# Optimization experiments

Measured on AMD Instinct MI355X. Metric: run time of the kernel, lower is better.

## Reference

```python
import math
import jax, jax.numpy as jnp
import numpy as np

N = 100000      # nodes
E = 3200000     # edges (avg degree 32)
NFEAT = 512
NH = 256
NC = 40
NL = 8
ALPHA = 0.1
LAMDA = 0.5


def setup_inputs() -> dict:
    key = jax.random.key(0)
    ks = jax.random.split(key, 9)
    features = jax.random.normal(ks[0], (N, NFEAT), jnp.float32)
    edge_rows = jax.random.randint(ks[1], (E,), 0, N, jnp.int32)
    edge_cols = jax.random.randint(ks[2], (E,), 0, N, jnp.int32)
    # scale by 1/avg_degree so aggregated features stay O(1) (mimics normalized adjacency)
    edge_vals = jax.random.uniform(ks[3], (E,), jnp.float32) / 32.0
    # fcs[0]: nn.Linear(nfeat, nhidden) default init U(-1/sqrt(in), 1/sqrt(in))
    b1 = 1.0 / math.sqrt(NFEAT)
    W_in = jax.random.uniform(ks[4], (NFEAT, NH), jnp.float32, -b1, b1)
    b_in = jax.random.uniform(ks[5], (NH,), jnp.float32, -b1, b1)
    # GraphConvolution weights: U(-1/sqrt(out), 1/sqrt(out))
    bw = 1.0 / math.sqrt(NH)
    conv_weights = jax.random.uniform(ks[6], (NL, NH, NH), jnp.float32, -bw, bw)
    # fcs[1]: nn.Linear(nhidden, nclass)
    b2 = 1.0 / math.sqrt(NH)
    W_out = jax.random.uniform(ks[7], (NH, NC), jnp.float32, -b2, b2)
    b_out = jax.random.uniform(ks[8], (NC,), jnp.float32, -b2, b2)
    return {
        "features": features,
        "edge_rows": edge_rows,
        "edge_cols": edge_cols,
        "edge_vals": edge_vals,
        "W_in": W_in,
        "b_in": b_in,
        "conv_weights": conv_weights,
        "W_out": W_out,
        "b_out": b_out,
    }


def reference(features, edge_rows, edge_cols, edge_vals, W_in, b_in, conv_weights, W_out, b_out):
    # dropout p=0 in eval -> identity
    h = jax.nn.relu(features @ W_in + b_in)  # [N, NH]
    h0 = h
    for i in range(NL):
        theta = math.log(LAMDA / (i + 1) + 1.0)
        # SpMM: hi = G @ h via gather + segment-sum over destination rows
        hi = jax.ops.segment_sum(edge_vals[:, None] * h[edge_cols], edge_rows, num_segments=N)
        support = (1.0 - ALPHA) * hi + ALPHA * h0  # variant=False -> r == support
        h = jax.nn.relu(theta * (support @ conv_weights[i]) + (1.0 - theta) * support)
    return h @ W_out + b_out  # [N, NC]
```

## Files before the change

kernel.cpp:

```cpp
#include <hip/hip_runtime.h>
#include <hip/hip_fp16.h>
#include <math.h>

#define NNODE   100000
#define NEDGE   3200000
#define NFEAT   512
#define NH      256
#define NC      40
#define NL      8

#define SCAN_B  256

typedef _Float16 f16x8 __attribute__((ext_vector_type(8)));
typedef float    f32x4 __attribute__((ext_vector_type(4)));

__global__ void count_deg_kernel(const int* __restrict__ rows, int* __restrict__ deg, int e) {
    int i = blockIdx.x * blockDim.x + threadIdx.x;
    if (i < e) atomicAdd(&deg[rows[i]], 1);
}

__global__ void scan_pass1(const int* __restrict__ deg, int* __restrict__ rowptr,
                           int* __restrict__ bsums, int n) {
    __shared__ int sm[SCAN_B];
    int i = blockIdx.x * SCAN_B + threadIdx.x;
    int v = (i < n) ? deg[i] : 0;
    sm[threadIdx.x] = v;
    __syncthreads();
    for (int off = 1; off < SCAN_B; off <<= 1) {
        int t = (threadIdx.x >= (unsigned)off) ? sm[threadIdx.x - off] : 0;
        __syncthreads();
        sm[threadIdx.x] += t;
        __syncthreads();
    }
    if (i < n) rowptr[i] = sm[threadIdx.x] - v;
    if (threadIdx.x == SCAN_B - 1) bsums[blockIdx.x] = sm[threadIdx.x];
}

__global__ void scan_pass2(int* __restrict__ bsums, int nb) {
    __shared__ int sm[512];
    int tid = threadIdx.x;
    int v = (tid < nb) ? bsums[tid] : 0;
    sm[tid] = v;
    __syncthreads();
    for (int off = 1; off < 512; off <<= 1) {
        int t = (tid >= off) ? sm[tid - off] : 0;
        __syncthreads();
        sm[tid] += t;
        __syncthreads();
    }
    if (tid < nb) bsums[tid] = sm[tid] - v;
}

__global__ void scan_pass3(int* __restrict__ rowptr, const int* __restrict__ bsums,
                           int* __restrict__ cursor, int n, int total) {
    int i = blockIdx.x * blockDim.x + threadIdx.x;
    if (i < n) {
        int v = rowptr[i] + bsums[i / SCAN_B];
        rowptr[i] = v;
        cursor[i] = v;
    }
    if (i == 0) rowptr[n] = total;
}

__global__ void scatter_edges_kernel(const int* __restrict__ rows, const int* __restrict__ cols,
                                     const float* __restrict__ vals, int* __restrict__ cursor,
                                     unsigned* __restrict__ csr_pk, int e) {
    int i = blockIdx.x * blockDim.x + threadIdx.x;
    if (i < e) {
        int r = rows[i];
        int p = atomicAdd(&cursor[r], 1);
        int q = (int)rintf(vals[i] * 1048576.0f);
        if (q > 32767) q = 32767;
        csr_pk[p] = ((unsigned)cols[i] << 15) | (unsigned)q;
    }
}

__device__ inline float4 dec8(uint2 p) {
    __half2 h01 = *(__half2*)&p.x;
    __half2 h23 = *(__half2*)&p.y;
    float2 f01 = __half22float2(h01);
    float2 f23 = __half22float2(h23);
    return make_float4(f01.x, f01.y, f23.x, f23.y);
}

__device__ inline void gload16(const void* g, void* l) {
    __builtin_amdgcn_global_load_lds((const __attribute__((address_space(1))) void*)g,
                                     (__attribute__((address_space(3))) void*)l,
                                     16, 0, 0);
}

#define VAL_SCALE 9.5367431640625e-7f

__global__ void convert_win(const float* __restrict__ in, __half* __restrict__ out) {
    int idx = blockIdx.x * blockDim.x + threadIdx.x;
    if (idx < NFEAT * NH) {
        int k = idx >> 8;
        int n = idx & 255;
        out[n * NFEAT + k] = __float2half(in[idx]);
    }
}

__global__ void convert_convw(const float* __restrict__ in, __half* __restrict__ out) {
    int idx = blockIdx.x * blockDim.x + threadIdx.x;
    if (idx < NL * NH * NH) {
        int l = idx >> 16;
        int rem = idx & 65535;
        int k = rem >> 8;
        int n = rem & 255;
        out[(size_t)l * 65536 + n * 256 + k] = __float2half(in[idx]);
    }
}

__global__ void convert_wout(const float* __restrict__ in, __half* __restrict__ out) {
    int idx = blockIdx.x * blockDim.x + threadIdx.x;
    if (idx < 64 * 256) {
        int ncol = idx >> 8;
        int k    = idx & 255;
        out[idx] = (ncol < NC) ? __float2half(in[k * NC + ncol]) : __float2half(0.f);
    }
}

__global__ __launch_bounds__(256) void spmm_full(
    const int* __restrict__ rowptr, const unsigned* __restrict__ csr_pk,
    const __half* __restrict__ h16, const __half* __restrict__ h016,
    __half* __restrict__ sup16, int n)
{
    int lane = threadIdx.x & 63;
    int r = blockIdx.x * 4 + (threadIdx.x >> 6);
    if (r >= n) return;
    int e0 = rowptr[r], e1 = rowptr[r + 1];
    const uint2* hv = (const uint2*)h16;
    float4 acc = make_float4(0.f, 0.f, 0.f, 0.f);
    int e = e0;
    #pragma unroll 1
    for (; e + 8 <= e1; e += 8) {
        unsigned a[8];
        uint2 p[8];
        #pragma unroll
        for (int j = 0; j < 8; ++j) a[j] = csr_pk[e + j];
        #pragma unroll
        for (int j = 0; j < 8; ++j) p[j] = hv[(size_t)(a[j] >> 15) * 64 + lane];
        #pragma unroll
        for (int j = 0; j < 8; ++j) {
            float v = (float)(a[j] & 32767u) * VAL_SCALE;
            float4 x = dec8(p[j]);
            acc.x += v * x.x; acc.y += v * x.y;
            acc.z += v * x.z; acc.w += v * x.w;
        }
    }
    #pragma unroll 1
    for (; e < e1; ++e) {
        unsigned a = csr_pk[e];
        float v = (float)(a & 32767u) * VAL_SCALE;
        float4 x = dec8(hv[(size_t)(a >> 15) * 64 + lane]);
        acc.x += v * x.x; acc.y += v * x.y; acc.z += v * x.z; acc.w += v * x.w;
    }
    float4 s0 = dec8(((const uint2*)h016)[(size_t)r * 64 + lane]);
    float4 o;
    o.x = 0.9f * acc.x + 0.1f * s0.x;
    o.y = 0.9f * acc.y + 0.1f * s0.y;
    o.z = 0.9f * acc.z + 0.1f * s0.z;
    o.w = 0.9f * acc.w + 0.1f * s0.w;
    __half2 ha = __floats2half2_rn(o.x, o.y);
    __half2 hb = __floats2half2_rn(o.z, o.w);
    uint2 pk;
    pk.x = *(unsigned*)&ha;
    pk.y = *(unsigned*)&hb;
    ((uint2*)sup16)[(size_t)r * 64 + lane] = pk;
}

__global__ __launch_bounds__(256) void spmm_half(
    const int* __restrict__ rowptr, const unsigned* __restrict__ csr_pk,
    const __half* __restrict__ h16, const __half* __restrict__ h016,
    __half* __restrict__ sup16, int n, int uoff)
{
    int lane = threadIdx.x & 63;
    int r = blockIdx.x * 4 + (threadIdx.x >> 6);
    if (r >= n) return;
    int e0 = rowptr[r], e1 = rowptr[r + 1];
    const unsigned* hv = (const unsigned*)h16;
    float2 acc = make_float2(0.f, 0.f);
    int e = e0;
    #pragma unroll 1
    for (; e + 8 <= e1; e += 8) {
        unsigned a[8], p[8];
        #pragma unroll
        for (int j = 0; j < 8; ++j) a[j] = csr_pk[e + j];
        #pragma unroll
        for (int j = 0; j < 8; ++j) p[j] = hv[(size_t)(a[j] >> 15) * 128 + uoff + lane];
        #pragma unroll
        for (int j = 0; j < 8; ++j) {
            float v = (float)(a[j] & 32767u) * VAL_SCALE;
            float2 x = __half22float2(*(__half2*)&p[j]);
            acc.x += v * x.x; acc.y += v * x.y;
        }
    }
    #pragma unroll 1
    for (; e < e1; ++e) {
        unsigned a = csr_pk[e];
        float v = (float)(a & 32767u) * VAL_SCALE;
        unsigned pw = hv[(size_t)(a >> 15) * 128 + uoff + lane];
        float2 x = __half22float2(*(__half2*)&pw);
        acc.x += v * x.x; acc.y += v * x.y;
    }
    unsigned s0w = ((const unsigned*)h016)[(size_t)r * 128 + uoff + lane];
    float2 s0 = __half22float2(*(__half2*)&s0w);
    float2 o;
    o.x = 0.9f * acc.x + 0.1f * s0.x;
    o.y = 0.9f * acc.y + 0.1f * s0.y;
    __half2 hh = __floats2half2_rn(o.x, o.y);
    ((unsigned*)sup16)[(size_t)r * 128 + uoff + lane] = *(unsigned*)&hh;
}

template <bool AFLOAT>
__global__ __launch_bounds__(512) void mfma_gemm(
    const void* __restrict__ Aptr, const __half* __restrict__ BT,
    const float* __restrict__ bias, const __half* __restrict__ Csrc16,
    __half* __restrict__ out16, int M, int K,
    float theta, float omt, int mode)
{
    __shared__ __align__(16) char smem[49152];
    const int tid  = threadIdx.x;
    const int lane = tid & 63;
    const int w    = tid >> 6;
    const int wr   = w >> 2;
    const int wc   = w & 3;
    const int bm0  = blockIdx.x * 128;
    const size_t strideB = (size_t)K * 2;

    f32x4 acc[4][4];
    #pragma unroll
    for (int m = 0; m < 4; ++m)
        #pragma unroll
        for (int n = 0; n < 4; ++n)
            acc[m][n] = (f32x4)0.f;

    auto stage = [&](int kt, int buf) {
        char* base = smem + buf * 24576;
        const long k0b = (long)kt * 64;
        if constexpr (AFLOAT) {
            const float* A32 = (const float*)Aptr;
            #pragma unroll
            for (int it = 0; it < 2; ++it) {
                int idx = tid + it * 512;
                int r   = idx >> 3;
                int t   = idx & 7;
                int grow = bm0 + r; if (grow >= M) grow = M - 1;
                float4 f = *(const float4*)&A32[(size_t)grow * K + kt * 32 + t * 4];
                __half2 a = __floats2half2_rn(f.x, f.y);
                __half2 b = __floats2half2_rn(f.z, f.w);
                uint2 pk;
                pk.x = *(unsigned*)&a;
                pk.y = *(unsigned*)&b;
                int slot = t >> 1;
                int off  = r * 64 + ((slot ^ ((r >> 1) & 3)) << 4) + (t & 1) * 8;
                *(uint2*)(base + off) = pk;
            }
        } else {
            const char* A16 = (const char*)Aptr;
            int row = w * 16 + (lane >> 2);
            int q   = (lane & 3) * 16;
            int qs  = q ^ (((row >> 1) & 3) << 4);
            int grow = bm0 + row; if (grow >= M) grow = M - 1;
            gload16(A16 + (size_t)grow * strideB + k0b + qs, base + w * 1024);
        }
        #pragma unroll
        for (int i = 0; i < 2; ++i) {
            int ia  = w * 2 + i;
            int row = ia * 16 + (lane >> 2);
            int q   = (lane & 3) * 16;
            int qs  = q ^ (((row >> 1) & 3) << 4);
            gload16((const char*)BT + (size_t)row * strideB + k0b + qs,
                    base + 8192 + ia * 1024);
        }
    };

    auto compute = [&](int buf) {
        const char* As = smem + buf * 24576;
        const char* Bs = As + 8192;
        const int q = (lane >> 4) * 16;
        f16x8 af[4], bf[4];
        #pragma unroll
        for (int m = 0; m < 4; ++m) {
            int row = wr * 64 + m * 16 + (lane & 15);
            af[m] = *(const f16x8*)(As + row * 64 + (q ^ (((row >> 1) & 3) << 4)));
        }
        #pragma unroll
        for (int n = 0; n < 4; ++n) {
            int col = wc * 64 + n * 16 + (lane & 15);
            bf[n] = *(const f16x8*)(Bs + col * 64 + (q ^ (((col >> 1) & 3) << 4)));
        }
        #pragma unroll
        for (int m = 0; m < 4; ++m)
            #pragma unroll
            for (int n = 0; n < 4; ++n)
                acc[m][n] = __builtin_amdgcn_mfma_f32_16x16x32_f16(af[m], bf[n], acc[m][n], 0, 0, 0);
    };

    const int nkt = K >> 5;
    stage(0, 0);
    __syncthreads();
    for (int kt = 0; kt < nkt; ++kt) {
        if (kt + 1 < nkt) stage(kt + 1, (kt + 1) & 1);
        compute(kt & 1);
        __syncthreads();
    }

    #pragma unroll
    for (int m = 0; m < 4; ++m) {
        int rbase = bm0 + wr * 64 + m * 16 + (lane >> 4) * 4;
        #pragma unroll
        for (int r = 0; r < 4; ++r) {
            int grow = rbase + r;
            if (grow >= M) continue;
            #pragma unroll
            for (int n = 0; n < 4; ++n) {
                int gcol = wc * 64 + n * 16 + (lane & 15);
                float x = acc[m][n][r];
                if (mode == 0) {
                    x = fmaxf(x + bias[gcol], 0.f);
                } else {
                    float s = __half2float(Csrc16[(size_t)grow * 256 + gcol]);
                    x = fmaxf(theta * x + omt * s, 0.f);
                }
                out16[(size_t)grow * 256 + gcol] = __float2half(x);
            }
        }
    }
}

__global__ __launch_bounds__(256) void mfma_out(
    const __half* __restrict__ A16, const __half* __restrict__ BT,
    const float* __restrict__ bias, float* __restrict__ out32, int M)
{
    __shared__ __align__(16) char smem[40960];
    const int tid  = threadIdx.x;
    const int lane = tid & 63;
    const int w    = tid >> 6;
    const int bm0  = blockIdx.x * 256;

    f32x4 acc[4][4];
    #pragma unroll
    for (int m = 0; m < 4; ++m)
        #pragma unroll
        for (int n = 0; n < 4; ++n)
            acc[m][n] = (f32x4)0.f;

    auto stage = [&](int kt, int buf) {
        char* base = smem + buf * 20480;
        const long k0b = (long)kt * 64;
        #pragma unroll
        for (int i = 0; i < 4; ++i) {
            int ia  = w * 4 + i;
            int row = ia * 16 + (lane >> 2);
            int q   = (lane & 3) * 16;
            int qs  = q ^ (((row >> 1) & 3) << 4);
            int grow = bm0 + row; if (grow >= M) grow = M - 1;
            gload16((const char*)A16 + (size_t)grow * 512 + k0b + qs, base + ia * 1024);
        }
        {
            int row = w * 16 + (lane >> 2);
            int q   = (lane & 3) * 16;
            int qs  = q ^ (((row >> 1) & 3) << 4);
            gload16((const char*)BT + (size_t)row * 512 + k0b + qs,
                    base + 16384 + w * 1024);
        }
    };

    auto compute = [&](int buf) {
        const char* As = smem + buf * 20480;
        const char* Bs = As + 16384;
        const int q = (lane >> 4) * 16;
        f16x8 af[4], bf[4];
        #pragma unroll
        for (int m = 0; m < 4; ++m) {
            int row = w * 64 + m * 16 + (lane & 15);
            af[m] = *(const f16x8*)(As + row * 64 + (q ^ (((row >> 1) & 3) << 4)));
        }
        #pragma unroll
        for (int n = 0; n < 4; ++n) {
            int col = n * 16 + (lane & 15);
            bf[n] = *(const f16x8*)(Bs + col * 64 + (q ^ (((col >> 1) & 3) << 4)));
        }
        #pragma unroll
        for (int m = 0; m < 4; ++m)
            #pragma unroll
            for (int n = 0; n < 4; ++n)
                acc[m][n] = __builtin_amdgcn_mfma_f32_16x16x32_f16(af[m], bf[n], acc[m][n], 0, 0, 0);
    };

    stage(0, 0);
    __syncthreads();
    for (int kt = 0; kt < 8; ++kt) {
        if (kt + 1 < 8) stage(kt + 1, (kt + 1) & 1);
        compute(kt & 1);
        __syncthreads();
    }

    #pragma unroll
    for (int m = 0; m < 4; ++m) {
        int rbase = bm0 + w * 64 + m * 16 + (lane >> 4) * 4;
        #pragma unroll
        for (int r = 0; r < 4; ++r) {
            int grow = rbase + r;
            if (grow >= M) continue;
            #pragma unroll
            for (int n = 0; n < 3; ++n) {
                int gcol = n * 16 + (lane & 15);
                if (gcol < NC)
                    out32[(size_t)grow * NC + gcol] = acc[m][n][r] + bias[gcol];
            }
        }
    }
}

extern "C" void kernel_launch(void* const* d_in, const int* in_sizes, int n_in,
                              void* d_out, int out_size, void* d_ws, size_t ws_size,
                              hipStream_t stream) {
    const float* features = (const float*)d_in[0];
    const int*   erows    = (const int*)d_in[1];
    const int*   ecols    = (const int*)d_in[2];
    const float* evals    = (const float*)d_in[3];
    const float* W_in     = (const float*)d_in[4];
    const float* b_in     = (const float*)d_in[5];
    const float* convW    = (const float*)d_in[6];
    const float* W_out    = (const float*)d_in[7];
    const float* b_out    = (const float*)d_in[8];
    float* out = (float*)d_out;

    const int n = NNODE;
    const int e = NEDGE;

    char* w = (char*)d_ws;
    auto alloc = [&](size_t bytes) -> void* {
        void* p = (void*)w;
        w += (bytes + 255) & ~(size_t)255;
        return p;
    };
    __half*   h0_16    = (__half*)alloc((size_t)n * NH * 2);
    __half*   hb_16    = (__half*)alloc((size_t)n * NH * 2);
    __half*   sup16    = (__half*)alloc((size_t)n * NH * 2);
    __half*   WtIn16   = (__half*)alloc((size_t)NFEAT * NH * 2);
    __half*   convWt16 = (__half*)alloc((size_t)NL * NH * NH * 2);
    __half*   WtOut16  = (__half*)alloc((size_t)64 * NH * 2);
    int*      rowptr   = (int*)alloc((size_t)(n + 1) * 4);
    int*      cursor   = (int*)alloc((size_t)n * 4);
    int*      bsums    = (int*)alloc(4096 * 4);
    unsigned* csr_pk   = (unsigned*)alloc((size_t)e * 4);

    convert_win<<<(NFEAT * NH + 255) / 256, 256, 0, stream>>>(W_in, WtIn16);
    convert_convw<<<(NL * NH * NH + 255) / 256, 256, 0, stream>>>(convW, convWt16);
    convert_wout<<<(64 * 256 + 255) / 256, 256, 0, stream>>>(W_out, WtOut16);

    hipMemsetAsync(cursor, 0, (size_t)n * 4, stream);
    count_deg_kernel<<<(e + 255) / 256, 256, 0, stream>>>(erows, cursor, e);
    int nb = (n + SCAN_B - 1) / SCAN_B;
    scan_pass1<<<nb, SCAN_B, 0, stream>>>(cursor, rowptr, bsums, n);
    scan_pass2<<<1, 512, 0, stream>>>(bsums, nb);
    scan_pass3<<<nb, SCAN_B, 0, stream>>>(rowptr, bsums, cursor, n, e);
    scatter_edges_kernel<<<(e + 255) / 256, 256, 0, stream>>>(
        erows, ecols, evals, cursor, csr_pk, e);

    dim3 gmm((n + 127) / 128, 1);
    mfma_gemm<true><<<gmm, 512, 0, stream>>>(features, WtIn16, b_in, nullptr,
                                             h0_16, n, NFEAT, 0.f, 0.f, 0);

    const __half* hcur16 = h0_16;
    for (int i = 0; i < NL; ++i) {
        if ((i & 1) == 0) {
            spmm_full<<<(n + 3) / 4, 256, 0, stream>>>(rowptr, csr_pk,
                                                       hcur16, h0_16, sup16, n);
        } else {
            spmm_half<<<(n + 3) / 4, 256, 0, stream>>>(rowptr, csr_pk,
                                                       hcur16, h0_16, sup16, n, 0);
            spmm_half<<<(n + 3) / 4, 256, 0, stream>>>(rowptr, csr_pk,
                                                       hcur16, h0_16, sup16, n, 64);
        }
        double th = log(0.5 / (double)(i + 1) + 1.0);
        mfma_gemm<false><<<gmm, 512, 0, stream>>>(sup16, convWt16 + (size_t)i * NH * NH,
                                                  nullptr, sup16, hb_16,
                                                  n, NH, (float)th, (float)(1.0 - th), 1);
        hcur16 = hb_16;
    }

    mfma_out<<<(n + 255) / 256, 256, 0, stream>>>(hb_16, WtOut16, b_out, out, n);
}
```

Baseline: 2.923 ms.

## Bucket CSR edges by column block and sweep SpMM rows per column band

Edges are now sorted within each row into 25 column buckets of 4096 nodes, which requires a per-row, per-bucket count, scan and scatter. A new SpMM kernel gives each wavefront 25 rows and walks all of them through one column bucket at a time, so that gathers from the feature matrix stay inside a small band that can stay cache-resident. Every layer now uses two half-width launches instead of alternating full and half kernels. The price is a larger preprocessing cost, 25 register accumulators per lane, and loss of the 8-way unrolled gather loop, since each row-bucket segment holds only about one edge and the latency is poorly hidden.

Result: slower. 8.657 ms (+196.2%).

```diff
diff --git a/kernel.cpp b/kernel.cpp
--- a/kernel.cpp
+++ b/kernel.cpp
@@ -10,20 +10,32 @@
 #define NL      8
 
 #define SCAN_B  256
+#define NB      25
+#define RPW     25
+#define RPB     100
+#define PBLK    1024
 
 typedef _Float16 f16x8 __attribute__((ext_vector_type(8)));
 typedef float    f32x4 __attribute__((ext_vector_type(4)));
 
-__global__ void count_deg_kernel(const int* __restrict__ rows, int* __restrict__ deg, int e) {
+#define VAL_SCALE 9.5367431640625e-7f
+
+__global__ void cnt2_kernel(const int* __restrict__ rows, const int* __restrict__ cols,
+                            int* __restrict__ cnt2, int e) {
     int i = blockIdx.x * blockDim.x + threadIdx.x;
-    if (i < e) atomicAdd(&deg[rows[i]], 1);
-}
-
-__global__ void scan_pass1(const int* __restrict__ deg, int* __restrict__ rowptr,
+    if (i < e) atomicAdd(&cnt2[rows[i] * NB + (cols[i] >> 12)], 1);
+}
+
+__global__ void scan_pass1(const int* __restrict__ cnt2, int* __restrict__ rowptr,
                            int* __restrict__ bsums, int n) {
     __shared__ int sm[SCAN_B];
     int i = blockIdx.x * SCAN_B + threadIdx.x;
-    int v = (i < n) ? deg[i] : 0;
+    int v = 0;
+    if (i < n) {
+        const int* c = &cnt2[i * NB];
+        #pragma unroll
+        for (int b = 0; b < NB; ++b) v += c[b];
+    }
     sm[threadIdx.x] = v;
     __syncthreads();
     for (int off = 1; off < SCAN_B; off <<= 1) {
@@ -51,27 +63,39 @@
     if (tid < nb) bsums[tid] = sm[tid] - v;
 }
 
-__global__ void scan_pass3(int* __restrict__ rowptr, const int* __restrict__ bsums,
-                           int* __restrict__ cursor, int n, int total) {
+__global__ void scan_pass3(int* __restrict__ rowptr, const int* __restrict__ bsums, int n) {
     int i = blockIdx.x * blockDim.x + threadIdx.x;
-    if (i < n) {
-        int v = rowptr[i] + bsums[i / SCAN_B];
-        rowptr[i] = v;
-        cursor[i] = v;
-    }
-    if (i == 0) rowptr[n] = total;
-}
-
-__global__ void scatter_edges_kernel(const int* __restrict__ rows, const int* __restrict__ cols,
-                                     const float* __restrict__ vals, int* __restrict__ cursor,
-                                     unsigned* __restrict__ csr_pk, int e) {
+    if (i < n) rowptr[i] += bsums[i / SCAN_B];
+}
+
+__global__ void rowptr2_kernel(const int* __restrict__ rowptr, const int* __restrict__ cnt2,
+                               int* __restrict__ rowptr2, int* __restrict__ cursor2,
+                               int n, int e) {
+    int r = blockIdx.x * blockDim.x + threadIdx.x;
+    if (r < n) {
+        int run = rowptr[r];
+        const int* c = &cnt2[r * NB];
+        #pragma unroll
+        for (int b = 0; b < NB; ++b) {
+            rowptr2[r * NB + b] = run;
+            cursor2[r * NB + b] = run;
+            run += c[b];
+        }
+    }
+    if (r == 0) rowptr2[(size_t)n * NB] = e;
+}
+
+__global__ void scatter2_kernel(const int* __restrict__ rows, const int* __restrict__ cols,
+                                const float* __restrict__ vals, int* __restrict__ cursor2,
+                                unsigned* __restrict__ csr_pk, int e) {
     int i = blockIdx.x * blockDim.x + threadIdx.x;
     if (i < e) {
         int r = rows[i];
-        int p = atomicAdd(&cursor[r], 1);
+        int c = cols[i];
+        int p = atomicAdd(&cursor2[r * NB + (c >> 12)], 1);
         int q = (int)rintf(vals[i] * 1048576.0f);
         if (q > 32767) q = 32767;
-        csr_pk[p] = ((unsigned)cols[i] << 15) | (unsigned)q;
+        csr_pk[p] = ((unsigned)c << 15) | (unsigned)q;
     }
 }
 
@@ -88,8 +112,6 @@
                                      (__attribute__((address_space(3))) void*)l,
                                      16, 0, 0);
 }
-
-#define VAL_SCALE 9.5367431640625e-7f
 
 __global__ void convert_win(const float* __restrict__ in, __half* __restrict__ out) {
     int idx = blockIdx.x * blockDim.x + threadIdx.x;
@@ -120,96 +142,61 @@
     }
 }
 
-__global__ __launch_bounds__(256) void spmm_full(
-    const int* __restrict__ rowptr, const unsigned* __restrict__ csr_pk,
-    const __half* __restrict__ h16, const __half* __restrict__ h016,
-    __half* __restrict__ sup16, int n)
-{
-    int lane = threadIdx.x & 63;
-    int r = blockIdx.x * 4 + (threadIdx.x >> 6);
-    if (r >= n) return;
-    int e0 = rowptr[r], e1 = rowptr[r + 1];
-    const uint2* hv = (const uint2*)h16;
-    float4 acc = make_float4(0.f, 0.f, 0.f, 0.f);
-    int e = e0;
-    #pragma unroll 1
-    for (; e + 8 <= e1; e += 8) {
-        unsigned a[8];
-        uint2 p[8];
-        #pragma unroll
-        for (int j = 0; j < 8; ++j) a[j] = csr_pk[e + j];
-        #pragma unroll
-        for (int j = 0; j < 8; ++j) p[j] = hv[(size_t)(a[j] >> 15) * 64 + lane];
-        #pragma unroll
-        for (int j = 0; j < 8; ++j) {
-            float v = (float)(a[j] & 32767u) * VAL_SCALE;
-            float4 x = dec8(p[j]);
-            acc.x += v * x.x; acc.y += v * x.y;
-            acc.z += v * x.z; acc.w += v * x.w;
-        }
-    }
-    #pragma unroll 1
-    for (; e < e1; ++e) {
-        unsigned a = csr_pk[e];
-        float v = (float)(a & 32767u) * VAL_SCALE;
-        float4 x = dec8(hv[(size_t)(a >> 15) * 64 + lane]);
-        acc.x += v * x.x; acc.y += v * x.y; acc.z += v * x.z; acc.w += v * x.w;
-    }
-    float4 s0 = dec8(((const uint2*)h016)[(size_t)r * 64 + lane]);
-    float4 o;
-    o.x = 0.9f * acc.x + 0.1f * s0.x;
-    o.y = 0.9f * acc.y + 0.1f * s0.y;
-    o.z = 0.9f * acc.z + 0.1f * s0.z;
-    o.w = 0.9f * acc.w + 0.1f * s0.w;
-    __half2 ha = __floats2half2_rn(o.x, o.y);
-    __half2 hb = __floats2half2_rn(o.z, o.w);
-    uint2 pk;
-    pk.x = *(unsigned*)&ha;
-    pk.y = *(unsigned*)&hb;
-    ((uint2*)sup16)[(size_t)r * 64 + lane] = pk;
-}
-
-__global__ __launch_bounds__(256) void spmm_half(
-    const int* __restrict__ rowptr, const unsigned* __restrict__ csr_pk,
+__global__ __launch_bounds__(256, 4) void spmm_pers(
+    const int* __restrict__ rowptr2, const unsigned* __restrict__ csr_pk,
     const __half* __restrict__ h16, const __half* __restrict__ h016,
     __half* __restrict__ sup16, int n, int uoff)
 {
-    int lane = threadIdx.x & 63;
-    int r = blockIdx.x * 4 + (threadIdx.x >> 6);
-    if (r >= n) return;
-    int e0 = rowptr[r], e1 = rowptr[r + 1];
+    __shared__ int bnd[RPB * NB + 1];
+    const int tid   = threadIdx.x;
+    const int lane  = tid & 63;
+    const int widx  = tid >> 6;
+    const int r0blk = blockIdx.x * RPB;
+    const int jmax  = n * NB;
+    for (int j = tid; j <= RPB * NB; j += 256) {
+        int g = r0blk * NB + j;
+        bnd[j] = rowptr2[g > jmax ? jmax : g];
+    }
+    __syncthreads();
+
+    const int fo = uoff + lane;
     const unsigned* hv = (const unsigned*)h16;
-    float2 acc = make_float2(0.f, 0.f);
-    int e = e0;
-    #pragma unroll 1
-    for (; e + 8 <= e1; e += 8) {
-        unsigned a[8], p[8];
-        #pragma unroll
-        for (int j = 0; j < 8; ++j) a[j] = csr_pk[e + j];
-        #pragma unroll
-        for (int j = 0; j < 8; ++j) p[j] = hv[(size_t)(a[j] >> 15) * 128 + uoff + lane];
-        #pragma unroll
-        for (int j = 0; j < 8; ++j) {
-            float v = (float)(a[j] & 32767u) * VAL_SCALE;
-            float2 x = __half22float2(*(__half2*)&p[j]);
-            acc.x += v * x.x; acc.y += v * x.y;
-        }
-    }
-    #pragma unroll 1
-    for (; e < e1; ++e) {
-        unsigned a = csr_pk[e];
-        float v = (float)(a & 32767u) * VAL_SCALE;
-        unsigned pw = hv[(size_t)(a >> 15) * 128 + uoff + lane];
-        float2 x = __half22float2(*(__half2*)&pw);
-        acc.x += v * x.x; acc.y += v * x.y;
-    }
-    unsigned s0w = ((const unsigned*)h016)[(size_t)r * 128 + uoff + lane];
-    float2 s0 = __half22float2(*(__half2*)&s0w);
-    float2 o;
-    o.x = 0.9f * acc.x + 0.1f * s0.x;
-    o.y = 0.9f * acc.y + 0.1f * s0.y;
-    __half2 hh = __floats2half2_rn(o.x, o.y);
-    ((unsigned*)sup16)[(size_t)r * 128 + uoff + lane] = *(unsigned*)&hh;
+    const int lr0 = widx * RPW;
+
+    float2 acc[RPW];
+    #pragma unroll
+    for (int i = 0; i < RPW; ++i) acc[i] = make_float2(0.f, 0.f);
+
+    for (int b = 0; b < NB; ++b) {
+        #pragma unroll
+        for (int i = 0; i < RPW; ++i) {
+            int gr = r0blk + lr0 + i;
+            if (gr >= n) continue;
+            int e0 = bnd[(lr0 + i) * NB + b];
+            int e1 = bnd[(lr0 + i) * NB + b + 1];
+            for (int e = e0; e < e1; ++e) {
+                unsigned a = csr_pk[e];
+                float v = (float)(a & 32767u) * VAL_SCALE;
+                unsigned pw = hv[(size_t)(a >> 15) * 128 + fo];
+                float2 x = __half22float2(*(__half2*)&pw);
+                acc[i].x += v * x.x;
+                acc[i].y += v * x.y;
+            }
+        }
+    }
+
+    #pragma unroll
+    for (int i = 0; i < RPW; ++i) {
+        int gr = r0blk + lr0 + i;
+        if (gr >= n) continue;
+        unsigned s0w = ((const unsigned*)h016)[(size_t)gr * 128 + fo];
+        float2 s0 = __half22float2(*(__half2*)&s0w);
+        float2 o;
+        o.x = 0.9f * acc[i].x + 0.1f * s0.x;
+        o.y = 0.9f * acc[i].y + 0.1f * s0.y;
+        __half2 hh = __floats2half2_rn(o.x, o.y);
+        ((unsigned*)sup16)[(size_t)gr * 128 + fo] = *(unsigned*)&hh;
+    }
 }
 
 template <bool AFLOAT>
@@ -444,22 +431,25 @@
     __half*   convWt16 = (__half*)alloc((size_t)NL * NH * NH * 2);
     __half*   WtOut16  = (__half*)alloc((size_t)64 * NH * 2);
     int*      rowptr   = (int*)alloc((size_t)(n + 1) * 4);
-    int*      cursor   = (int*)alloc((size_t)n * 4);
     int*      bsums    = (int*)alloc(4096 * 4);
+    int*      cnt2     = (int*)alloc((size_t)n * NB * 4);
+    int*      rowptr2  = (int*)alloc(((size_t)n * NB + 1) * 4);
+    int*      cursor2  = (int*)alloc((size_t)n * NB * 4);
     unsigned* csr_pk   = (unsigned*)alloc((size_t)e * 4);
 
     convert_win<<<(NFEAT * NH + 255) / 256, 256, 0, stream>>>(W_in, WtIn16);
     convert_convw<<<(NL * NH * NH + 255) / 256, 256, 0, stream>>>(convW, convWt16);
     convert_wout<<<(64 * 256 + 255) / 256, 256, 0, stream>>>(W_out, WtOut16);
 
-    hipMemsetAsync(cursor, 0, (size_t)n * 4, stream);
-    count_deg_kernel<<<(e + 255) / 256, 256, 0, stream>>>(erows, cursor, e);
+    hipMemsetAsync(cnt2, 0, (size_t)n * NB * 4, stream);
+    cnt2_kernel<<<(e + 255) / 256, 256, 0, stream>>>(erows, ecols, cnt2, e);
     int nb = (n + SCAN_B - 1) / SCAN_B;
-    scan_pass1<<<nb, SCAN_B, 0, stream>>>(cursor, rowptr, bsums, n);
+    scan_pass1<<<nb, SCAN_B, 0, stream>>>(cnt2, rowptr, bsums, n);
     scan_pass2<<<1, 512, 0, stream>>>(bsums, nb);
-    scan_pass3<<<nb, SCAN_B, 0, stream>>>(rowptr, bsums, cursor, n, e);
-    scatter_edges_kernel<<<(e + 255) / 256, 256, 0, stream>>>(
-        erows, ecols, evals, cursor, csr_pk, e);
+    scan_pass3<<<nb, SCAN_B, 0, stream>>>(rowptr, bsums, n);
+    rowptr2_kernel<<<(n + 255) / 256, 256, 0, stream>>>(rowptr, cnt2, rowptr2, cursor2, n, e);
+    scatter2_kernel<<<(e + 255) / 256, 256, 0, stream>>>(erows, ecols, evals, cursor2,
+                                                         csr_pk, e);
 
     dim3 gmm((n + 127) / 128, 1);
     mfma_gemm<true><<<gmm, 512, 0, stream>>>(features, WtIn16, b_in, nullptr,
@@ -467,15 +457,8 @@
 
     const __half* hcur16 = h0_16;
     for (int i = 0; i < NL; ++i) {
-        if ((i & 1) == 0) {
-            spmm_full<<<(n + 3) / 4, 256, 0, stream>>>(rowptr, csr_pk,
-                                                       hcur16, h0_16, sup16, n);
-        } else {
-            spmm_half<<<(n + 3) / 4, 256, 0, stream>>>(rowptr, csr_pk,
-                                                       hcur16, h0_16, sup16, n, 0);
-            spmm_half<<<(n + 3) / 4, 256, 0, stream>>>(rowptr, csr_pk,
-                                                       hcur16, h0_16, sup16, n, 64);
-        }
+        spmm_pers<<<PBLK, 256, 0, stream>>>(rowptr2, csr_pk, hcur16, h0_16, sup16, n, 0);
+        spmm_pers<<<PBLK, 256, 0, stream>>>(rowptr2, csr_pk, hcur16, h0_16, sup16, n, 64);
         double th = log(0.5 / (double)(i + 1) + 1.0);
         mfma_gemm<false><<<gmm, 512, 0, stream>>>(sup16, convWt16 + (size_t)i * NH * NH,
                                                   nullptr, sup16, hb_16,
```
